# Optimization experiments

Measured on AMD Instinct MI355X. Metric: run time of the kernel, lower is better.

## Reference

```python
import jax, jax.numpy as jnp
import numpy as np

N_EXPERTS = 8
TOP_K = 2
D_MODEL = 1024
HIDDEN = 4096          # shared expert hidden
ROUTED_H = 1024        # hidden // expert_scale
BATCH, SEQ = 2, 4096


def setup_inputs() -> dict:
    key = jax.random.key(0)
    ks = jax.random.split(key, 8)
    std = 0.02
    return {
        "x": jax.random.normal(ks[0], (BATCH, SEQ, D_MODEL), dtype=jnp.float32),
        "w12": std * jax.random.normal(ks[1], (N_EXPERTS, 2 * ROUTED_H, D_MODEL), dtype=jnp.float32),
        "w3": std * jax.random.normal(ks[2], (N_EXPERTS, D_MODEL, ROUTED_H), dtype=jnp.float32),
        "shared_w1": std * jax.random.normal(ks[3], (HIDDEN, D_MODEL), dtype=jnp.float32),
        "shared_w2": std * jax.random.normal(ks[4], (HIDDEN, D_MODEL), dtype=jnp.float32),
        "shared_w3": std * jax.random.normal(ks[5], (D_MODEL, HIDDEN), dtype=jnp.float32),
        "router_w": std * jax.random.normal(ks[6], (N_EXPERTS, D_MODEL), dtype=jnp.float32),
        "expert_bias": jnp.zeros((N_EXPERTS,), dtype=jnp.float32),
    }


def reference(x, w12, w3, shared_w1, shared_w2, shared_w3, router_w, expert_bias):
    b, s, d = x.shape
    xf = x.reshape(-1, d)  # (T, d)

    # shared expert: SwiGLU
    shared = (jax.nn.silu(xf @ shared_w1.T) * (xf @ shared_w2.T)) @ shared_w3.T

    # router: sigmoid scores, bias-adjusted selection, gather scores at top-k
    scores = jax.nn.sigmoid(xf @ router_w.T)            # (T, E)
    _, top_idx = jax.lax.top_k(scores + expert_bias, TOP_K)  # (T, k)
    mask = jax.nn.one_hot(top_idx, N_EXPERTS, dtype=xf.dtype).sum(axis=-2)  # (T, E)
    gates = scores * mask                               # routing weights (0 for unselected)

    # routed experts: SwiGLU with per-expert weights, combined by gates.
    # Equivalent to sort/dispatch/grouped-GEMM/scatter of the original.
    h12 = jnp.einsum('td,ehd->teh', xf, w12)            # (T, E, 2H)
    h1, h2 = jnp.split(h12, 2, axis=-1)
    h = jax.nn.silu(h1) * h2 * gates[:, :, None]        # (T, E, H)
    routed = jnp.einsum('teh,edh->td', h, w3)           # (T, d)

    return (shared + routed).reshape(b, s, d)
```

## Files before the change

### kernel.cpp

```cpp
#include <hip/hip_runtime.h>

typedef unsigned short u16;
typedef __bf16 bf16x8 __attribute__((ext_vector_type(8)));
typedef float f32x4 __attribute__((ext_vector_type(4)));

#define TOK 8192
#define DM 1024
#define HID 4096
#define RH 1024
#define NE 8
#define MAX_SLOTS 17408

__device__ __forceinline__ u16 f2bf(float f) {
  union { float f; unsigned u; } v; v.f = f;
  unsigned u = v.u;
  return (u16)((u + 0x7fffu + ((u >> 16) & 1u)) >> 16);
}

struct alignas(8) U16x4 { u16 x, y, z, w; };

__global__ __launch_bounds__(256) void k_cast4(const float4* __restrict__ in, U16x4* __restrict__ out, int n4) {
  int i = blockIdx.x * 256 + threadIdx.x;
  if (i >= n4) return;
  float4 v = in[i];
  out[i] = U16x4{f2bf(v.x), f2bf(v.y), f2bf(v.z), f2bf(v.w)};
}

__global__ __launch_bounds__(256) void k_pack_shared(const float4* __restrict__ w1, const float4* __restrict__ w2,
                                                     U16x4* __restrict__ out) {
  int i = blockIdx.x * 256 + threadIdx.x;
  int row = i >> 8, c4 = i & 255;
  const float4* src = (row & 1) ? w2 : w1;
  float4 v = src[(size_t)(row >> 1) * 256 + c4];
  out[(size_t)row * 256 + c4] = U16x4{f2bf(v.x), f2bf(v.y), f2bf(v.z), f2bf(v.w)};
}

__global__ __launch_bounds__(256) void k_pack_routed(const float4* __restrict__ w12, U16x4* __restrict__ out) {
  int i = blockIdx.x * 256 + threadIdx.x;
  int c4 = i & 255;
  int row = (i >> 8) & 2047;
  int e = i >> 19;
  int srow = (row & 1) ? (1024 + (row >> 1)) : (row >> 1);
  float4 v = w12[((size_t)e * 2048 + srow) * 256 + c4];
  out[((size_t)e * 2048 + row) * 256 + c4] = U16x4{f2bf(v.x), f2bf(v.y), f2bf(v.z), f2bf(v.w)};
}

__global__ __launch_bounds__(256) void k_router(const float* __restrict__ x, const float* __restrict__ rw,
                                                const float* __restrict__ bias,
                                                int* __restrict__ tok_e, float* __restrict__ tok_g) {
  int wave = threadIdx.x >> 6, lane = threadIdx.x & 63;
  int t = blockIdx.x * 4 + wave;
  const float4* xr = (const float4*)(x + (size_t)t * DM) + lane * 4;
  float4 xv[4];
#pragma unroll
  for (int j = 0; j < 4; j++) xv[j] = xr[j];
  float p[NE];
#pragma unroll
  for (int e = 0; e < NE; e++) {
    const float4* wr = (const float4*)(rw + (size_t)e * DM) + lane * 4;
    float s = 0.f;
#pragma unroll
    for (int j = 0; j < 4; j++) {
      float4 w = wr[j];
      s += xv[j].x * w.x + xv[j].y * w.y + xv[j].z * w.z + xv[j].w * w.w;
    }
    p[e] = s;
  }
#pragma unroll
  for (int e = 0; e < NE; e++) {
    float v = p[e];
#pragma unroll
    for (int off = 32; off; off >>= 1) v += __shfl_xor(v, off, 64);
    p[e] = v;
  }
  if (lane == 0) {
    float sc[NE];
#pragma unroll
    for (int e = 0; e < NE; e++) sc[e] = 1.f / (1.f + __expf(-p[e]));
    int e0 = 0; float b0 = sc[0] + bias[0];
#pragma unroll
    for (int e = 1; e < NE; e++) { float v = sc[e] + bias[e]; if (v > b0) { b0 = v; e0 = e; } }
    int e1 = -1; float b1 = -1e30f;
#pragma unroll
    for (int e = 0; e < NE; e++) { if (e == e0) continue; float v = sc[e] + bias[e]; if (v > b1) { b1 = v; e1 = e; } }
    tok_e[t * 2] = e0; tok_e[t * 2 + 1] = e1;
    tok_g[t * 2] = sc[e0]; tok_g[t * 2 + 1] = sc[e1];
  }
}

__global__ __launch_bounds__(256) void k_count(const int* __restrict__ tok_e, int* __restrict__ counts) {
  __shared__ int cnt[NE];
  int tid = threadIdx.x;
  if (tid < NE) cnt[tid] = 0;
  __syncthreads();
  int t = blockIdx.x * 256 + tid;
  atomicAdd(&cnt[tok_e[t * 2]], 1);
  atomicAdd(&cnt[tok_e[t * 2 + 1]], 1);
  __syncthreads();
  if (tid < NE) atomicAdd(&counts[tid], cnt[tid]);
}

__global__ void k_offsets(const int* __restrict__ counts, int* __restrict__ offs) {
  int o = 0;
#pragma unroll
  for (int e = 0; e < NE; e++) {
    offs[e] = o;
    o += (counts[e] + 127) & ~127;
  }
  offs[NE] = o;
}

__global__ __launch_bounds__(256) void k_init_slots(int* __restrict__ slot_token, float* __restrict__ slot_gate) {
  int i = blockIdx.x * 256 + threadIdx.x;
  if (i < MAX_SLOTS) { slot_token[i] = 0; slot_gate[i] = 0.f; }
}

__global__ __launch_bounds__(256) void k_assign(const int* __restrict__ tok_e, const float* __restrict__ tok_g,
                                                const int* __restrict__ offs, int* __restrict__ cursors,
                                                int* __restrict__ slot_token, float* __restrict__ slot_gate,
                                                int* __restrict__ token_slots) {
  __shared__ int lcnt[NE];
  __shared__ int base[NE];
  int tid = threadIdx.x;
  if (tid < NE) lcnt[tid] = 0;
  __syncthreads();
  int t = blockIdx.x * 256 + tid;
  int e0 = tok_e[t * 2], e1 = tok_e[t * 2 + 1];
  int r0 = atomicAdd(&lcnt[e0], 1);
  int r1 = atomicAdd(&lcnt[e1], 1);
  __syncthreads();
  if (tid < NE) base[tid] = atomicAdd(&cursors[tid], lcnt[tid]);
  __syncthreads();
  int s0 = offs[e0] + base[e0] + r0;
  int s1 = offs[e1] + base[e1] + r1;
  slot_token[s0] = t;
  slot_gate[s0] = tok_g[t * 2];
  token_slots[t * 2] = s0;
  slot_token[s1] = t;
  slot_gate[s1] = tok_g[t * 2 + 1];
  token_slots[t * 2 + 1] = s1;
}

#define AS1(p) ((__attribute__((address_space(1))) void*)(p))
#define AS3(p) ((__attribute__((address_space(3))) void*)(p))

template<int EPI, bool GROUPED, bool GATHER, bool GATE>
__global__ __launch_bounds__(256, 2) void gemm_bt(
    const u16* __restrict__ A, int lda,
    const u16* __restrict__ B, int ldb, size_t strideB,
    void* __restrict__ Cout, int ldc,
    int M, int N, int K,
    const int* __restrict__ slot_token,
    const float* __restrict__ slot_gate,
    const int* __restrict__ counts,
    const int* __restrict__ offs) {
  __shared__ alignas(16) u16 Al[128 * 64];
  __shared__ alignas(16) u16 Bl[128 * 64];
  const int tid = threadIdx.x;
  const int lane = tid & 63, wave = tid >> 6;
  const int nt = blockIdx.x, mt = blockIdx.y;
  int m0g;
  const u16* Bp = B;
  if (GROUPED) {
    const int e = blockIdx.z;
    int cnt = counts[e];
    if (mt * 128 >= cnt) return;
    m0g = offs[e] + mt * 128;
    Bp += (size_t)e * strideB;
  } else {
    m0g = mt * 128;
  }
  const int n0 = nt * 128;

  const u16* aSrc[4];
  const u16* bSrc[4];
#pragma unroll
  for (int j = 0; j < 4; j++) {
    int r = wave * 32 + j * 8 + (lane >> 3);
    int cg = (lane & 7) ^ (r & 7);
    int arow;
    if (GROUPED) {
      int slot = m0g + r;
      arow = GATHER ? slot_token[slot] : slot;
    } else {
      arow = m0g + r;
    }
    aSrc[j] = A + (size_t)arow * lda + cg * 8;
    bSrc[j] = Bp + (size_t)(n0 + r) * ldb + cg * 8;
  }

  f32x4 acc[4][4];
#pragma unroll
  for (int m = 0; m < 4; m++)
#pragma unroll
    for (int n = 0; n < 4; n++) acc[m][n] = (f32x4){0.f, 0.f, 0.f, 0.f};

  const int wm = wave >> 1, wn = wave & 1;
  const int KT = K >> 6;
  for (int kt = 0; kt < KT; ++kt) {
    __syncthreads();
#pragma unroll
    for (int j = 0; j < 4; j++) {
      __builtin_amdgcn_global_load_lds(AS1(aSrc[j]), AS3(&Al[(wave * 32 + j * 8) * 64]), 16, 0, 0);
      __builtin_amdgcn_global_load_lds(AS1(bSrc[j]), AS3(&Bl[(wave * 32 + j * 8) * 64]), 16, 0, 0);
      aSrc[j] += 64; bSrc[j] += 64;
    }
    asm volatile("s_waitcnt vmcnt(0)" ::: "memory");
    __syncthreads();
#pragma unroll
    for (int ks = 0; ks < 2; ++ks) {
      bf16x8 af[4], bfv[4];
#pragma unroll
      for (int m = 0; m < 4; m++) {
        int row = wm * 64 + m * 16 + (lane & 15);
        int cg = ((lane >> 4) + ks * 4) ^ (row & 7);
        af[m] = *(const bf16x8*)&Al[row * 64 + cg * 8];
      }
#pragma unroll
      for (int n = 0; n < 4; n++) {
        int row = wn * 64 + n * 16 + (lane & 15);
        int cg = ((lane >> 4) + ks * 4) ^ (row & 7);
        bfv[n] = *(const bf16x8*)&Bl[row * 64 + cg * 8];
      }
#pragma unroll
      for (int m = 0; m < 4; m++)
#pragma unroll
        for (int n = 0; n < 4; n++)
          acc[m][n] = __builtin_amdgcn_mfma_f32_16x16x32_bf16(af[m], bfv[n], acc[m][n], 0, 0, 0);
    }
  }

  if (EPI == 2) {
    float* Cf = (float*)Cout;
#pragma unroll
    for (int m = 0; m < 4; m++) {
#pragma unroll
      for (int r = 0; r < 4; r++) {
        int row = wm * 64 + m * 16 + (lane >> 4) * 4 + r;
        size_t grow = (size_t)(m0g + row);
#pragma unroll
        for (int n = 0; n < 4; n++) {
          int col = n0 + wn * 64 + n * 16 + (lane & 15);
          Cf[grow * ldc + col] = acc[m][n][r];
        }
      }
    }
  } else {
    u16* Cb = (u16*)Cout;
#pragma unroll
    for (int m = 0; m < 4; m++) {
#pragma unroll
      for (int r = 0; r < 4; r++) {
        int row = wm * 64 + m * 16 + (lane >> 4) * 4 + r;
        int grow = m0g + row;
        float gate = 1.f;
        if (GATE) gate = slot_gate[grow];
#pragma unroll
        for (int n = 0; n < 4; n++) {
          float v = acc[m][n][r];
          float o = __shfl_xor(v, 1, 64);
          if (!(lane & 1)) {
            float g = v / (1.f + __expf(-v)) * o * gate;
            int col = (n0 + wn * 64 + n * 16 + (lane & 15)) >> 1;
            Cb[(size_t)grow * ldc + col] = f2bf(g);
          }
        }
      }
    }
  }
}

__global__ __launch_bounds__(256) void k_combine(float4* __restrict__ out, const float4* __restrict__ rp,
                                                 const int* __restrict__ token_slots) {
  int i = blockIdx.x * 256 + threadIdx.x;
  int t = i >> 8, c4 = i & 255;
  int s0 = token_slots[t * 2], s1 = token_slots[t * 2 + 1];
  float4 a = out[i];
  float4 b = rp[(size_t)s0 * 256 + c4];
  float4 c = rp[(size_t)s1 * 256 + c4];
  a.x += b.x + c.x; a.y += b.y + c.y; a.z += b.z + c.z; a.w += b.w + c.w;
  out[i] = a;
}

extern "C" void kernel_launch(void* const* d_in, const int* in_sizes, int n_in,
                              void* d_out, int out_size, void* d_ws, size_t ws_size,
                              hipStream_t stream) {
  const float* x    = (const float*)d_in[0];
  const float* w12  = (const float*)d_in[1];
  const float* w3   = (const float*)d_in[2];
  const float* sw1  = (const float*)d_in[3];
  const float* sw2  = (const float*)d_in[4];
  const float* sw3  = (const float*)d_in[5];
  const float* rw   = (const float*)d_in[6];
  const float* bias = (const float*)d_in[7];
  float* out = (float*)d_out;

  char* ws = (char*)d_ws;
  size_t off = 0;
  auto alloc = [&](size_t bytes) -> void* {
    void* p = ws + off;
    off += (bytes + 255) & ~(size_t)255;
    return p;
  };
  u16* xb   = (u16*)alloc((size_t)TOK * DM * 2);
  u16* wshu = (u16*)alloc((size_t)2 * HID * DM * 2);
  u16* wshd = (u16*)alloc((size_t)DM * HID * 2);
  u16* wru  = (u16*)alloc((size_t)NE * 2 * RH * DM * 2);
  u16* wrd  = (u16*)alloc((size_t)NE * DM * RH * 2);
  u16* gr   = (u16*)alloc((size_t)MAX_SLOTS * RH * 2);
  void* gunion = alloc((size_t)MAX_SLOTS * RH * 4);
  u16* g    = (u16*)gunion;
  float* rp = (float*)gunion;
  int* cc      = (int*)alloc(64);
  int* counts  = cc;
  int* cursors = cc + 8;
  int* offs    = (int*)alloc(16 * 4);
  int* tok_e   = (int*)alloc((size_t)TOK * 2 * 4);
  float* tok_g = (float*)alloc((size_t)TOK * 2 * 4);
  int* slot_token  = (int*)alloc((size_t)MAX_SLOTS * 4);
  float* slot_gate = (float*)alloc((size_t)MAX_SLOTS * 4);
  int* token_slots = (int*)alloc((size_t)TOK * 2 * 4);
  (void)in_sizes; (void)n_in; (void)out_size; (void)ws_size;

  hipMemsetAsync(cc, 0, 64, stream);
  k_cast4<<<8192, 256, 0, stream>>>((const float4*)x, (U16x4*)xb, TOK * DM / 4);
  k_pack_shared<<<8192, 256, 0, stream>>>((const float4*)sw1, (const float4*)sw2, (U16x4*)wshu);
  k_cast4<<<4096, 256, 0, stream>>>((const float4*)sw3, (U16x4*)wshd, DM * HID / 4);
  k_pack_routed<<<16384, 256, 0, stream>>>((const float4*)w12, (U16x4*)wru);
  k_cast4<<<8192, 256, 0, stream>>>((const float4*)w3, (U16x4*)wrd, NE * DM * RH / 4);
  k_init_slots<<<(MAX_SLOTS + 255) / 256, 256, 0, stream>>>(slot_token, slot_gate);
  k_router<<<TOK / 4, 256, 0, stream>>>(x, rw, bias, tok_e, tok_g);
  k_count<<<TOK / 256, 256, 0, stream>>>(tok_e, counts);
  k_offsets<<<1, 1, 0, stream>>>(counts, offs);
  k_assign<<<TOK / 256, 256, 0, stream>>>(tok_e, tok_g, offs, cursors, slot_token, slot_gate, token_slots);

  gemm_bt<1, false, false, false><<<dim3(64, 64, 1), 256, 0, stream>>>(
      xb, DM, wshu, DM, 0, g, HID, TOK, 2 * HID, DM, nullptr, nullptr, nullptr, nullptr);
  gemm_bt<2, false, false, false><<<dim3(8, 64, 1), 256, 0, stream>>>(
      g, HID, wshd, HID, 0, out, DM, TOK, DM, HID, nullptr, nullptr, nullptr, nullptr);
  gemm_bt<1, true, true, true><<<dim3(16, 64, 8), 256, 0, stream>>>(
      xb, DM, wru, DM, (size_t)2 * RH * DM, gr, RH, 0, 2 * RH, DM, slot_token, slot_gate, counts, offs);
  gemm_bt<2, true, false, false><<<dim3(8, 64, 8), 256, 0, stream>>>(
      gr, RH, wrd, RH, (size_t)DM * RH, rp, DM, 0, DM, RH, nullptr, nullptr, counts, offs);

  k_combine<<<TOK, 256, 0, stream>>>((float4*)out, (const float4*)rp, token_slots);
}
```

Baseline: 540.4 us.

## Add 256x256 eight-wave ping-pong GEMM for shared and routed up-projections

Adds a new gemm8p kernel with 512 threads, 256x256 tiles, double-buffered LDS with direct global-to-LDS loads, and an interleaved quadrant schedule that splits MFMA work between barriers. It is used for the shared-expert and routed-expert up-projection GEMMs, the latter with the gather and gate epilogue. The shared GEMM also gets an XCD-aware block swizzle. To match the larger tile, routed expert segments are padded to 256 slots and MAX_SLOTS grows, which adds padding work to the routed GEMMs. The aim is higher arithmetic intensity and better MFMA utilisation in the largest GEMMs, at the cost of more LDS and register pressure.

```diff
diff --git a/kernel.cpp b/kernel.cpp
--- a/kernel.cpp
+++ b/kernel.cpp
@@ -9,7 +9,7 @@
 #define HID 4096
 #define RH 1024
 #define NE 8
-#define MAX_SLOTS 17408
+#define MAX_SLOTS 18432
 
 __device__ __forceinline__ u16 f2bf(float f) {
   union { float f; unsigned u; } v; v.f = f;
@@ -18,6 +18,7 @@
 }
 
 struct alignas(8) U16x4 { u16 x, y, z, w; };
+template<int V> struct IC { static constexpr int v = V; };
 
 __global__ __launch_bounds__(256) void k_cast4(const float4* __restrict__ in, U16x4* __restrict__ out, int n4) {
   int i = blockIdx.x * 256 + threadIdx.x;
@@ -105,7 +106,7 @@
 #pragma unroll
   for (int e = 0; e < NE; e++) {
     offs[e] = o;
-    o += (counts[e] + 127) & ~127;
+    o += (counts[e] + 255) & ~255;
   }
   offs[NE] = o;
 }
@@ -143,6 +144,217 @@
 
 #define AS1(p) ((__attribute__((address_space(1))) void*)(p))
 #define AS3(p) ((__attribute__((address_space(3))) void*)(p))
+
+template<int BN, int EPI, bool GROUPED, bool GATHER, bool GATE, bool XSWZ>
+__global__ __launch_bounds__(512, 2) void gemm8p(
+    const u16* __restrict__ A, int lda,
+    const u16* __restrict__ Bmat, int ldb, size_t strideB,
+    void* __restrict__ Cout, int ldc,
+    int KT,
+    const int* __restrict__ slot_token, const float* __restrict__ slot_gate,
+    const int* __restrict__ counts, const int* __restrict__ offs) {
+  constexpr int NR = BN / 64;
+  constexpr int NH = NR / 2;
+  constexpr int LB = BN / 128;
+  __shared__ alignas(16) u16 Al[2][256 * 64];
+  __shared__ alignas(16) u16 Bl[2][BN * 64];
+
+  const int tid = threadIdx.x;
+  const int lane = tid & 63, wave = tid >> 6;
+  const int wm = wave >> 2, wn = wave & 3;
+  const int l15 = lane & 15, l4h = lane >> 4, l7 = lane & 7;
+
+  int nt = blockIdx.x, mt = blockIdx.y;
+  if (XSWZ) {
+    int lin = mt * 32 + nt;
+    int swz = (lin & 7) * 128 + (lin >> 3);
+    nt = swz & 31; mt = swz >> 5;
+  }
+  int m0g;
+  const u16* Bp = Bmat;
+  if (GROUPED) {
+    const int e = blockIdx.z;
+    if (mt * 256 >= counts[e]) return;
+    m0g = offs[e] + mt * 256;
+    Bp += (size_t)e * strideB;
+  } else {
+    m0g = mt * 256;
+  }
+  const int n0 = nt * BN;
+
+  const int sro = wave * 8 + (lane >> 3);
+  const int cg = (lane & 7) ^ ((lane >> 3) & 7);
+  const u16* aP[2][2];
+#pragma unroll
+  for (int qm = 0; qm < 2; qm++)
+#pragma unroll
+    for (int j = 0; j < 2; j++) {
+      int lr = j * 128 + qm * 64 + sro;
+      int arow = m0g + lr;
+      if (GROUPED && GATHER) arow = slot_token[m0g + lr];
+      aP[qm][j] = A + (size_t)arow * lda + cg * 8;
+    }
+  const u16* bP[2][LB];
+#pragma unroll
+  for (int qn = 0; qn < 2; qn++)
+#pragma unroll
+    for (int j = 0; j < LB; j++) {
+      int rest = j * 64 + sro;
+      int brow = (NR == 4) ? ((rest >> 5) * 64 + qn * 32 + (rest & 31))
+                           : ((rest >> 4) * 32 + qn * 16 + (rest & 15));
+      bP[qn][j] = Bp + (size_t)(n0 + brow) * ldb + cg * 8;
+    }
+
+  f32x4 acc[8][NR];
+#pragma unroll
+  for (int m = 0; m < 8; m++)
+#pragma unroll
+    for (int n = 0; n < NR; n++) acc[m][n] = (f32x4){0.f, 0.f, 0.f, 0.f};
+  bf16x8 af[8], bq0[2 * NH], bq1[2 * NH];
+
+  auto stA = [&](auto bufc, auto qmc, int kt) {
+    constexpr int buf = decltype(bufc)::v, qm = decltype(qmc)::v;
+#pragma unroll
+    for (int j = 0; j < 2; j++)
+      __builtin_amdgcn_global_load_lds(AS1(aP[qm][j] + (size_t)kt * 64),
+                                       AS3(&Al[buf][(qm * 128 + j * 64 + wave * 8) * 64]), 16, 0, 0);
+  };
+  auto stB = [&](auto bufc, auto qnc, int kt) {
+    constexpr int buf = decltype(bufc)::v, qn = decltype(qnc)::v;
+#pragma unroll
+    for (int j = 0; j < LB; j++)
+      __builtin_amdgcn_global_load_lds(AS1(bP[qn][j] + (size_t)kt * 64),
+                                       AS3(&Bl[buf][(qn * (BN / 2) + j * 64 + wave * 8) * 64]), 16, 0, 0);
+  };
+  auto ldA = [&](auto bufc, auto qmc) {
+    constexpr int buf = decltype(bufc)::v, qm = decltype(qmc)::v;
+#pragma unroll
+    for (int mm = 0; mm < 4; mm++)
+#pragma unroll
+      for (int ks = 0; ks < 2; ks++) {
+        int p = qm * 128 + wm * 64 + mm * 16 + l15;
+        af[mm * 2 + ks] = *(const bf16x8*)&Al[buf][p * 64 + ((ks * 4 + l4h) ^ l7) * 8];
+      }
+  };
+  auto ldB = [&](auto bufc, auto qnc, bf16x8* bq) {
+    constexpr int buf = decltype(bufc)::v, qn = decltype(qnc)::v;
+#pragma unroll
+    for (int nn = 0; nn < NH; nn++)
+#pragma unroll
+      for (int ks = 0; ks < 2; ks++) {
+        int p = qn * (BN / 2) + wn * (NH * 16) + nn * 16 + l15;
+        bq[nn * 2 + ks] = *(const bf16x8*)&Bl[buf][p * 64 + ((ks * 4 + l4h) ^ l7) * 8];
+      }
+  };
+  auto quad = [&](auto qmc, auto qnc, bf16x8* bq) {
+    constexpr int qm = decltype(qmc)::v, qn = decltype(qnc)::v;
+    __builtin_amdgcn_s_setprio(1);
+#pragma unroll
+    for (int mm = 0; mm < 4; mm++)
+#pragma unroll
+      for (int nn = 0; nn < NH; nn++)
+#pragma unroll
+        for (int ks = 0; ks < 2; ks++)
+          acc[qm * 4 + mm][qn * NH + nn] = __builtin_amdgcn_mfma_f32_16x16x32_bf16(
+              af[mm * 2 + ks], bq[nn * 2 + ks], acc[qm * 4 + mm][qn * NH + nn], 0, 0, 0);
+    __builtin_amdgcn_s_setprio(0);
+  };
+  auto vmw = [&]() {
+    if constexpr (BN == 256) asm volatile("s_waitcnt vmcnt(4)" ::: "memory");
+    else                     asm volatile("s_waitcnt vmcnt(3)" ::: "memory");
+  };
+#define BAR() __builtin_amdgcn_s_barrier()
+
+  stA(IC<0>{}, IC<0>{}, 0); stB(IC<0>{}, IC<0>{}, 0);
+  stA(IC<0>{}, IC<1>{}, 0); stB(IC<0>{}, IC<1>{}, 0);
+  stA(IC<1>{}, IC<0>{}, 1); stB(IC<1>{}, IC<0>{}, 1);
+  vmw();
+  BAR();
+
+  for (int i = 0; i < KT / 2; i++) {
+    const int t1 = 2 * i + 1;
+    const int s0 = (2 * i + 2 < KT) ? 2 * i + 2 : KT - 1;
+    const int s1 = (2 * i + 3 < KT) ? 2 * i + 3 : KT - 1;
+    ldA(IC<0>{}, IC<0>{});
+    ldB(IC<0>{}, IC<0>{}, bq0);
+    stA(IC<1>{}, IC<1>{}, t1);
+    BAR();
+    quad(IC<0>{}, IC<0>{}, bq0);
+    BAR();
+    ldB(IC<0>{}, IC<1>{}, bq1);
+    stB(IC<1>{}, IC<1>{}, t1);
+    BAR();
+    quad(IC<0>{}, IC<1>{}, bq1);
+    BAR();
+    ldA(IC<0>{}, IC<1>{});
+    stA(IC<0>{}, IC<0>{}, s0);
+    BAR();
+    quad(IC<1>{}, IC<0>{}, bq0);
+    BAR();
+    stB(IC<0>{}, IC<0>{}, s0);
+    BAR();
+    quad(IC<1>{}, IC<1>{}, bq1);
+    vmw();
+    BAR();
+    ldA(IC<1>{}, IC<0>{});
+    ldB(IC<1>{}, IC<0>{}, bq0);
+    stA(IC<0>{}, IC<1>{}, s0);
+    BAR();
+    quad(IC<0>{}, IC<0>{}, bq0);
+    BAR();
+    ldB(IC<1>{}, IC<1>{}, bq1);
+    stB(IC<0>{}, IC<1>{}, s0);
+    BAR();
+    quad(IC<0>{}, IC<1>{}, bq1);
+    BAR();
+    ldA(IC<1>{}, IC<1>{});
+    stA(IC<1>{}, IC<0>{}, s1);
+    BAR();
+    quad(IC<1>{}, IC<0>{}, bq0);
+    BAR();
+    stB(IC<1>{}, IC<0>{}, s1);
+    BAR();
+    quad(IC<1>{}, IC<1>{}, bq1);
+    vmw();
+    BAR();
+  }
+#undef BAR
+
+  if (EPI == 2) {
+    float* Cf = (float*)Cout;
+#pragma unroll
+    for (int m = 0; m < 8; m++)
+#pragma unroll
+      for (int r = 0; r < 4; r++) {
+        size_t grow = (size_t)(m0g + wm * 128 + m * 16 + l4h * 4 + r);
+#pragma unroll
+        for (int n = 0; n < NR; n++) {
+          int col = n0 + wn * (NR * 16) + n * 16 + l15;
+          Cf[grow * ldc + col] = acc[m][n][r];
+        }
+      }
+  } else {
+    u16* Cb = (u16*)Cout;
+#pragma unroll
+    for (int m = 0; m < 8; m++)
+#pragma unroll
+      for (int r = 0; r < 4; r++) {
+        int grow = m0g + wm * 128 + m * 16 + l4h * 4 + r;
+        float gate = 1.f;
+        if (GATE) gate = slot_gate[grow];
+#pragma unroll
+        for (int n = 0; n < NR; n++) {
+          float v = acc[m][n][r];
+          float o = __shfl_xor(v, 1, 64);
+          if (!(lane & 1)) {
+            float g = v / (1.f + __expf(-v)) * o * gate;
+            int col = (n0 + wn * (NR * 16) + n * 16 + l15) >> 1;
+            Cb[(size_t)grow * ldc + col] = f2bf(g);
+          }
+        }
+      }
+  }
+}
 
 template<int EPI, bool GROUPED, bool GATHER, bool GATE>
 __global__ __launch_bounds__(256, 2) void gemm_bt(
@@ -334,12 +546,12 @@
   k_offsets<<<1, 1, 0, stream>>>(counts, offs);
   k_assign<<<TOK / 256, 256, 0, stream>>>(tok_e, tok_g, offs, cursors, slot_token, slot_gate, token_slots);
 
-  gemm_bt<1, false, false, false><<<dim3(64, 64, 1), 256, 0, stream>>>(
-      xb, DM, wshu, DM, 0, g, HID, TOK, 2 * HID, DM, nullptr, nullptr, nullptr, nullptr);
+  gemm8p<256, 1, false, false, false, true><<<dim3(32, 32, 1), 512, 0, stream>>>(
+      xb, DM, wshu, DM, 0, g, HID, 16, nullptr, nullptr, nullptr, nullptr);
+  gemm8p<256, 1, true, true, true, false><<<dim3(8, 32, 8), 512, 0, stream>>>(
+      xb, DM, wru, DM, (size_t)2 * RH * DM, gr, RH, 16, slot_token, slot_gate, counts, offs);
   gemm_bt<2, false, false, false><<<dim3(8, 64, 1), 256, 0, stream>>>(
       g, HID, wshd, HID, 0, out, DM, TOK, DM, HID, nullptr, nullptr, nullptr, nullptr);
-  gemm_bt<1, true, true, true><<<dim3(16, 64, 8), 256, 0, stream>>>(
-      xb, DM, wru, DM, (size_t)2 * RH * DM, gr, RH, 0, 2 * RH, DM, slot_token, slot_gate, counts, offs);
   gemm_bt<2, true, false, false><<<dim3(8, 64, 8), 256, 0, stream>>>(
       gr, RH, wrd, RH, (size_t)DM * RH, rp, DM, 0, DM, RH, nullptr, nullptr, counts, offs);
 
```

Measured after the change: 594.2 us. 9.9% more time.

## Fuse prep kernels, fold routed combine into shared down-proj epilogue, swizzle tiles

Applied to the files above, without the earlier changes.

Merges the five cast/pack kernels and the slot init into one prep launch. The routed down-projection now writes bf16 partials, and the shared down-projection GEMM epilogue gathers and adds each token's two routed partials, which removes the separate combine pass and the fp32 partial buffer. An XCD-aware block swizzle is added to the dense GEMMs, and expert padding grows to 256 rows with a larger grid. The cost is bf16 rounding of the routed partials, extra padded slots, and scattered gathers in the epilogue.

```diff
diff --git a/kernel.cpp b/kernel.cpp
--- a/kernel.cpp
+++ b/kernel.cpp
@@ -9,40 +9,52 @@
 #define HID 4096
 #define RH 1024
 #define NE 8
-#define MAX_SLOTS 17408
+#define MAX_SLOTS 18432
 
 __device__ __forceinline__ u16 f2bf(float f) {
   union { float f; unsigned u; } v; v.f = f;
   unsigned u = v.u;
   return (u16)((u + 0x7fffu + ((u >> 16) & 1u)) >> 16);
 }
+__device__ __forceinline__ float bf2f(u16 h) {
+  union { unsigned u; float f; } v; v.u = ((unsigned)h) << 16; return v.f;
+}
 
 struct alignas(8) U16x4 { u16 x, y, z, w; };
-
-__global__ __launch_bounds__(256) void k_cast4(const float4* __restrict__ in, U16x4* __restrict__ out, int n4) {
-  int i = blockIdx.x * 256 + threadIdx.x;
-  if (i >= n4) return;
-  float4 v = in[i];
-  out[i] = U16x4{f2bf(v.x), f2bf(v.y), f2bf(v.z), f2bf(v.w)};
-}
-
-__global__ __launch_bounds__(256) void k_pack_shared(const float4* __restrict__ w1, const float4* __restrict__ w2,
-                                                     U16x4* __restrict__ out) {
-  int i = blockIdx.x * 256 + threadIdx.x;
-  int row = i >> 8, c4 = i & 255;
-  const float4* src = (row & 1) ? w2 : w1;
-  float4 v = src[(size_t)(row >> 1) * 256 + c4];
-  out[(size_t)row * 256 + c4] = U16x4{f2bf(v.x), f2bf(v.y), f2bf(v.z), f2bf(v.w)};
-}
-
-__global__ __launch_bounds__(256) void k_pack_routed(const float4* __restrict__ w12, U16x4* __restrict__ out) {
-  int i = blockIdx.x * 256 + threadIdx.x;
-  int c4 = i & 255;
-  int row = (i >> 8) & 2047;
-  int e = i >> 19;
-  int srow = (row & 1) ? (1024 + (row >> 1)) : (row >> 1);
-  float4 v = w12[((size_t)e * 2048 + srow) * 256 + c4];
-  out[((size_t)e * 2048 + row) * 256 + c4] = U16x4{f2bf(v.x), f2bf(v.y), f2bf(v.z), f2bf(v.w)};
+__device__ __forceinline__ U16x4 cvt4(float4 v) {
+  return U16x4{f2bf(v.x), f2bf(v.y), f2bf(v.z), f2bf(v.w)};
+}
+
+__global__ __launch_bounds__(256) void k_prep(
+    const float4* __restrict__ x, const float4* __restrict__ sw1, const float4* __restrict__ sw2,
+    const float4* __restrict__ sw3, const float4* __restrict__ w12, const float4* __restrict__ w3,
+    U16x4* __restrict__ xb, U16x4* __restrict__ wshu, U16x4* __restrict__ wshd,
+    U16x4* __restrict__ wru, U16x4* __restrict__ wrd,
+    int* __restrict__ slot_token, float* __restrict__ slot_gate) {
+  int b = blockIdx.x, tid = threadIdx.x;
+  if (b < 8192) {
+    int i = b * 256 + tid;
+    xb[i] = cvt4(x[i]);
+  } else if (b < 16384) {
+    int i = (b - 8192) * 256 + tid;
+    int row = i >> 8, c4 = i & 255;
+    const float4* src = (row & 1) ? sw2 : sw1;
+    wshu[(size_t)row * 256 + c4] = cvt4(src[(size_t)(row >> 1) * 256 + c4]);
+  } else if (b < 20480) {
+    int i = (b - 16384) * 256 + tid;
+    wshd[i] = cvt4(sw3[i]);
+  } else if (b < 36864) {
+    int i = (b - 20480) * 256 + tid;
+    int c4 = i & 255, row = (i >> 8) & 2047, e = i >> 19;
+    int srow = (row & 1) ? (1024 + (row >> 1)) : (row >> 1);
+    wru[((size_t)e * 2048 + row) * 256 + c4] = cvt4(w12[((size_t)e * 2048 + srow) * 256 + c4]);
+  } else if (b < 45056) {
+    int i = (b - 36864) * 256 + tid;
+    wrd[i] = cvt4(w3[i]);
+  } else {
+    int i = (b - 45056) * 256 + tid;
+    if (i < MAX_SLOTS) { slot_token[i] = 0; slot_gate[i] = 0.f; }
+  }
 }
 
 __global__ __launch_bounds__(256) void k_router(const float* __restrict__ x, const float* __restrict__ rw,
@@ -105,14 +117,9 @@
 #pragma unroll
   for (int e = 0; e < NE; e++) {
     offs[e] = o;
-    o += (counts[e] + 127) & ~127;
+    o += (counts[e] + 255) & ~255;
   }
   offs[NE] = o;
-}
-
-__global__ __launch_bounds__(256) void k_init_slots(int* __restrict__ slot_token, float* __restrict__ slot_gate) {
-  int i = blockIdx.x * 256 + threadIdx.x;
-  if (i < MAX_SLOTS) { slot_token[i] = 0; slot_gate[i] = 0.f; }
 }
 
 __global__ __launch_bounds__(256) void k_assign(const int* __restrict__ tok_e, const float* __restrict__ tok_g,
@@ -144,21 +151,30 @@
 #define AS1(p) ((__attribute__((address_space(1))) void*)(p))
 #define AS3(p) ((__attribute__((address_space(3))) void*)(p))
 
-template<int EPI, bool GROUPED, bool GATHER, bool GATE>
+template<int EPI, bool GROUPED, bool GATHER, bool GATE, int XSWZ>
 __global__ __launch_bounds__(256, 2) void gemm_bt(
     const u16* __restrict__ A, int lda,
     const u16* __restrict__ B, int ldb, size_t strideB,
     void* __restrict__ Cout, int ldc,
-    int M, int N, int K,
+    int K,
     const int* __restrict__ slot_token,
     const float* __restrict__ slot_gate,
     const int* __restrict__ counts,
-    const int* __restrict__ offs) {
+    const int* __restrict__ offs,
+    const u16* __restrict__ rpb) {
   __shared__ alignas(16) u16 Al[128 * 64];
   __shared__ alignas(16) u16 Bl[128 * 64];
   const int tid = threadIdx.x;
   const int lane = tid & 63, wave = tid >> 6;
-  const int nt = blockIdx.x, mt = blockIdx.y;
+  int nt = blockIdx.x, mt = blockIdx.y;
+  if (XSWZ) {
+    int nx = gridDim.x;
+    int nwg = nx * gridDim.y;
+    int lin = mt * nx + nt;
+    int chunk = nwg >> 3;
+    int logical = (lin & 7) * chunk + (lin >> 3);
+    mt = logical / nx; nt = logical % nx;
+  }
   int m0g;
   const u16* Bp = B;
   if (GROUPED) {
@@ -230,18 +246,35 @@
     }
   }
 
-  if (EPI == 2) {
+  if (EPI == 4) {
     float* Cf = (float*)Cout;
 #pragma unroll
     for (int m = 0; m < 4; m++) {
 #pragma unroll
       for (int r = 0; r < 4; r++) {
-        int row = wm * 64 + m * 16 + (lane >> 4) * 4 + r;
-        size_t grow = (size_t)(m0g + row);
+        int grow = m0g + wm * 64 + m * 16 + (lane >> 4) * 4 + r;
+        int s0 = slot_token[grow * 2], s1 = slot_token[grow * 2 + 1];
+        const u16* p0 = rpb + (size_t)s0 * DM;
+        const u16* p1 = rpb + (size_t)s1 * DM;
 #pragma unroll
         for (int n = 0; n < 4; n++) {
           int col = n0 + wn * 64 + n * 16 + (lane & 15);
-          Cf[grow * ldc + col] = acc[m][n][r];
+          float v = acc[m][n][r] + bf2f(p0[col]) + bf2f(p1[col]);
+          Cf[(size_t)grow * ldc + col] = v;
+        }
+      }
+    }
+  } else if (EPI == 3) {
+    u16* Cb = (u16*)Cout;
+#pragma unroll
+    for (int m = 0; m < 4; m++) {
+#pragma unroll
+      for (int r = 0; r < 4; r++) {
+        int grow = m0g + wm * 64 + m * 16 + (lane >> 4) * 4 + r;
+#pragma unroll
+        for (int n = 0; n < 4; n++) {
+          int col = n0 + wn * 64 + n * 16 + (lane & 15);
+          Cb[(size_t)grow * ldc + col] = f2bf(acc[m][n][r]);
         }
       }
     }
@@ -251,8 +284,7 @@
     for (int m = 0; m < 4; m++) {
 #pragma unroll
       for (int r = 0; r < 4; r++) {
-        int row = wm * 64 + m * 16 + (lane >> 4) * 4 + r;
-        int grow = m0g + row;
+        int grow = m0g + wm * 64 + m * 16 + (lane >> 4) * 4 + r;
         float gate = 1.f;
         if (GATE) gate = slot_gate[grow];
 #pragma unroll
@@ -268,18 +300,6 @@
       }
     }
   }
-}
-
-__global__ __launch_bounds__(256) void k_combine(float4* __restrict__ out, const float4* __restrict__ rp,
-                                                 const int* __restrict__ token_slots) {
-  int i = blockIdx.x * 256 + threadIdx.x;
-  int t = i >> 8, c4 = i & 255;
-  int s0 = token_slots[t * 2], s1 = token_slots[t * 2 + 1];
-  float4 a = out[i];
-  float4 b = rp[(size_t)s0 * 256 + c4];
-  float4 c = rp[(size_t)s1 * 256 + c4];
-  a.x += b.x + c.x; a.y += b.y + c.y; a.z += b.z + c.z; a.w += b.w + c.w;
-  out[i] = a;
 }
 
 extern "C" void kernel_launch(void* const* d_in, const int* in_sizes, int n_in,
@@ -308,9 +328,8 @@
   u16* wru  = (u16*)alloc((size_t)NE * 2 * RH * DM * 2);
   u16* wrd  = (u16*)alloc((size_t)NE * DM * RH * 2);
   u16* gr   = (u16*)alloc((size_t)MAX_SLOTS * RH * 2);
-  void* gunion = alloc((size_t)MAX_SLOTS * RH * 4);
-  u16* g    = (u16*)gunion;
-  float* rp = (float*)gunion;
+  u16* g    = (u16*)alloc((size_t)TOK * HID * 2);
+  u16* rp   = (u16*)alloc((size_t)MAX_SLOTS * DM * 2);
   int* cc      = (int*)alloc(64);
   int* counts  = cc;
   int* cursors = cc + 8;
@@ -323,25 +342,21 @@
   (void)in_sizes; (void)n_in; (void)out_size; (void)ws_size;
 
   hipMemsetAsync(cc, 0, 64, stream);
-  k_cast4<<<8192, 256, 0, stream>>>((const float4*)x, (U16x4*)xb, TOK * DM / 4);
-  k_pack_shared<<<8192, 256, 0, stream>>>((const float4*)sw1, (const float4*)sw2, (U16x4*)wshu);
-  k_cast4<<<4096, 256, 0, stream>>>((const float4*)sw3, (U16x4*)wshd, DM * HID / 4);
-  k_pack_routed<<<16384, 256, 0, stream>>>((const float4*)w12, (U16x4*)wru);
-  k_cast4<<<8192, 256, 0, stream>>>((const float4*)w3, (U16x4*)wrd, NE * DM * RH / 4);
-  k_init_slots<<<(MAX_SLOTS + 255) / 256, 256, 0, stream>>>(slot_token, slot_gate);
+  k_prep<<<45128, 256, 0, stream>>>((const float4*)x, (const float4*)sw1, (const float4*)sw2,
+                                    (const float4*)sw3, (const float4*)w12, (const float4*)w3,
+                                    (U16x4*)xb, (U16x4*)wshu, (U16x4*)wshd, (U16x4*)wru, (U16x4*)wrd,
+                                    slot_token, slot_gate);
   k_router<<<TOK / 4, 256, 0, stream>>>(x, rw, bias, tok_e, tok_g);
   k_count<<<TOK / 256, 256, 0, stream>>>(tok_e, counts);
   k_offsets<<<1, 1, 0, stream>>>(counts, offs);
   k_assign<<<TOK / 256, 256, 0, stream>>>(tok_e, tok_g, offs, cursors, slot_token, slot_gate, token_slots);
 
-  gemm_bt<1, false, false, false><<<dim3(64, 64, 1), 256, 0, stream>>>(
-      xb, DM, wshu, DM, 0, g, HID, TOK, 2 * HID, DM, nullptr, nullptr, nullptr, nullptr);
-  gemm_bt<2, false, false, false><<<dim3(8, 64, 1), 256, 0, stream>>>(
-      g, HID, wshd, HID, 0, out, DM, TOK, DM, HID, nullptr, nullptr, nullptr, nullptr);
-  gemm_bt<1, true, true, true><<<dim3(16, 64, 8), 256, 0, stream>>>(
-      xb, DM, wru, DM, (size_t)2 * RH * DM, gr, RH, 0, 2 * RH, DM, slot_token, slot_gate, counts, offs);
-  gemm_bt<2, true, false, false><<<dim3(8, 64, 8), 256, 0, stream>>>(
-      gr, RH, wrd, RH, (size_t)DM * RH, rp, DM, 0, DM, RH, nullptr, nullptr, counts, offs);
-
-  k_combine<<<TOK, 256, 0, stream>>>((float4*)out, (const float4*)rp, token_slots);
-}
+  gemm_bt<1, false, false, false, 1><<<dim3(64, 64, 1), 256, 0, stream>>>(
+      xb, DM, wshu, DM, 0, g, HID, DM, nullptr, nullptr, nullptr, nullptr, nullptr);
+  gemm_bt<1, true, true, true, 0><<<dim3(16, 128, 8), 256, 0, stream>>>(
+      xb, DM, wru, DM, (size_t)2 * RH * DM, gr, RH, DM, slot_token, slot_gate, counts, offs, nullptr);
+  gemm_bt<3, true, false, false, 0><<<dim3(8, 128, 8), 256, 0, stream>>>(
+      gr, RH, wrd, RH, (size_t)DM * RH, rp, DM, RH, nullptr, nullptr, counts, offs, nullptr);
+  gemm_bt<4, false, false, false, 1><<<dim3(8, 64, 1), 256, 0, stream>>>(
+      g, HID, wshd, HID, 0, out, DM, HID, token_slots, nullptr, nullptr, nullptr, rp);
+}
```

New measurement: 513.8 us. 4.9% less time.
